# Optimization experiments

Measured on AMD Instinct MI355X. Metric: run time of the kernel, lower is better.

Reference implementation:

```python
import jax, jax.numpy as jnp
import numpy as np

# Standard NF4 quantization codebook (bitsandbytes values)
_NF4_CB = np.array([
    -1.0, -0.6961928009986877, -0.5250730514526367, -0.39491748809814453,
    -0.28444138169288635, -0.18477343022823334, -0.09105003625154495, 0.0,
    0.07958029955625534, 0.16093020141124725, 0.24611230194568634, 0.33791524171829224,
    0.44070982933044434, 0.5626170039176941, 0.7229568362236023, 1.0], dtype=np.float32)

B, L, H, E, DFF = 2, 2048, 2048, 8, 8192
BLK = 512  # NF4 quantization block size (b_idx = h // 512 in kernel)


def setup_inputs() -> dict:
    key = jax.random.key(0)
    ks = jax.random.split(key, 8)
    N = B * L
    x = jax.random.normal(ks[0], (B, L, H), dtype=jnp.float32)
    router_w = jax.random.normal(ks[1], (H, E), dtype=jnp.float32) * 0.02
    # packed NF4: one byte = two 4-bit codebook indices (low nibble -> even h)
    nf4 = jax.random.randint(ks[2], (N, E, H // 2), 0, 256, dtype=jnp.int32)
    mean = jax.random.normal(ks[3], (N, E, H // BLK), dtype=jnp.float32) * 0.01
    std = jax.random.uniform(ks[4], (N, E, H // BLK), dtype=jnp.float32) + 0.5
    codebook = jnp.asarray(_NF4_CB)
    w1 = jax.random.normal(ks[5], (H, DFF), dtype=jnp.float32) * 0.02
    w2 = jax.random.normal(ks[6], (DFF, H), dtype=jnp.float32) * 0.02
    return {"x": x, "router_w": router_w, "nf4": nf4, "mean": mean,
            "std": std, "codebook": codebook, "w1": w1, "w2": w2}


def reference(x, router_w, nf4, mean, std, codebook, w1, w2):
    b, l, h = x.shape
    n = b * l
    e = router_w.shape[1]
    xf = x.reshape(n, h)

    # shared expert MLP (base_mlp): Linear -> GELU -> Linear
    mlp = jax.nn.gelu(xf @ w1) @ w2  # [N, H]

    # router: logits in fp32, softmax, cast to fp16 as the kernel does
    logits = xf @ router_w  # [N, E]
    probs = jax.nn.softmax(logits, axis=-1).astype(jnp.float16).astype(jnp.float32)

    # NF4 unpack: low nibble -> even h, high nibble -> odd h
    low = nf4 & 15
    high = (nf4 >> 4) & 15
    idx = jnp.stack([low, high], axis=-1).reshape(n, e, h)  # interleave -> [N,E,H]
    vals = codebook[idx]  # codebook gather, [N,E,H]

    # per-block (512) rescale: val*std + mean
    nb = mean.shape[-1]
    blk = h // nb
    dq = (vals.reshape(n, e, nb, blk) * std[..., None] + mean[..., None]).reshape(n, e, h)

    # weighted expert mix + MLP residual add
    moe = jnp.einsum('ne,neh->nh', probs, dq)
    return (moe + mlp).reshape(b, l, h)
```

## Files before the change

### kernel.cpp

```cpp
#include <hip/hip_runtime.h>
#include <hip/hip_bf16.h>
#include <hip/hip_fp16.h>

#define H 2048
#define E 8
#define DFF 8192
#define NTOK 4096
#define NB 4

typedef _Float16 f16x8 __attribute__((ext_vector_type(8)));
typedef float f32x4 __attribute__((ext_vector_type(4)));

#define AS1 __attribute__((address_space(1)))
#define AS3 __attribute__((address_space(3)))

__device__ __forceinline__ void gl_lds16(const void* g, void* l) {
    __builtin_amdgcn_global_load_lds((const AS1 unsigned int*)g,
                                     (AS3 unsigned int*)l, 16, 0, 0);
}

__device__ __forceinline__ float gelu_f(float x) {
    float u = 0.7978845608028654f * x * (1.0f + 0.044715f * x * x);
    float t = fabsf(u);
    float e = __expf(-2.0f * t);
    float th = (1.0f - e) / (1.0f + e);
    th = copysignf(th, u);
    return 0.5f * x * (1.0f + th);
}

__global__ __launch_bounds__(256) void router_cast_kernel(
    const float* __restrict__ x, const float* __restrict__ rw,
    float* __restrict__ probs, _Float16* __restrict__ xh)
{
    int n = blockIdx.x, t = threadIdx.x;
    float acc[E];
#pragma unroll
    for (int e = 0; e < E; ++e) acc[e] = 0.f;
    const float* xr = x + (size_t)n * H;
#pragma unroll
    for (int k = 0; k < H / 256; ++k) {
        int h = t + k * 256;
        float xv = xr[h];
        xh[(size_t)n * H + h] = (_Float16)xv;
        const float4* r4 = reinterpret_cast<const float4*>(rw + (size_t)h * E);
        float4 a = r4[0], b = r4[1];
        acc[0] += xv * a.x; acc[1] += xv * a.y; acc[2] += xv * a.z; acc[3] += xv * a.w;
        acc[4] += xv * b.x; acc[5] += xv * b.y; acc[6] += xv * b.z; acc[7] += xv * b.w;
    }
#pragma unroll
    for (int e = 0; e < E; ++e) {
        float v = acc[e];
#pragma unroll
        for (int o = 32; o > 0; o >>= 1) v += __shfl_down(v, o, 64);
        acc[e] = v;
    }
    __shared__ float red[4][E];
    int wave = t >> 6, lane = t & 63;
    if (lane == 0) {
#pragma unroll
        for (int e = 0; e < E; ++e) red[wave][e] = acc[e];
    }
    __syncthreads();
    if (t == 0) {
        float lg[E];
        float mx = -1e30f;
#pragma unroll
        for (int e = 0; e < E; ++e) {
            lg[e] = red[0][e] + red[1][e] + red[2][e] + red[3][e];
            mx = fmaxf(mx, lg[e]);
        }
        float s = 0.f;
#pragma unroll
        for (int e = 0; e < E; ++e) { lg[e] = expf(lg[e] - mx); s += lg[e]; }
        float inv = 1.f / s;
#pragma unroll
        for (int e = 0; e < E; ++e) {
            float p = lg[e] * inv;
            p = __half2float(__float2half(p));
            probs[(size_t)n * E + e] = p;
        }
    }
}

__global__ __launch_bounds__(256) void transpose_cast_kernel(
    const float* __restrict__ src, _Float16* __restrict__ dst, int R, int C)
{
    __shared__ float tile[32][33];
    int tx = threadIdx.x & 31, ty = threadIdx.x >> 5;
    int c0 = blockIdx.x * 32, r0 = blockIdx.y * 32;
#pragma unroll
    for (int i = ty; i < 32; i += 8)
        tile[i][tx] = src[(size_t)(r0 + i) * C + c0 + tx];
    __syncthreads();
#pragma unroll
    for (int i = ty; i < 32; i += 8)
        dst[(size_t)(c0 + i) * R + r0 + tx] = (_Float16)tile[tx][i];
}

__global__ __launch_bounds__(256) void moe_kernel(
    const int* __restrict__ nf4, const float* __restrict__ mean,
    const float* __restrict__ stdv, const float* __restrict__ cb,
    const float* __restrict__ probs, float* __restrict__ moe)
{
    int n = blockIdx.x, t = threadIdx.x;
    __shared__ float cbl[32];
    __shared__ float ps[E][NB];
    __shared__ float cmean[NB];
    if (t < 16) { float v = cb[t]; cbl[t] = v; cbl[t + 16] = v; }
    else if (t >= 32 && t < 64) {
        int e = (t - 32) >> 2, b = t & 3;
        ps[e][b] = probs[(size_t)n * E + e] * stdv[((size_t)n * E + e) * NB + b];
    } else if (t >= 64 && t < 68) {
        int b = t - 64; float s = 0.f;
        for (int e = 0; e < E; ++e)
            s += probs[(size_t)n * E + e] * mean[((size_t)n * E + e) * NB + b];
        cmean[b] = s;
    }
    __syncthreads();
    int cboff = (t & 1) << 4;
    const int* w = nf4 + (size_t)n * (E * H / 2);
    float2* outp = reinterpret_cast<float2*>(moe + (size_t)n * H);
#pragma unroll
    for (int k = 0; k < 4; ++k) {
        int j = t + k * 256;
        float psr[E];
#pragma unroll
        for (int e = 0; e < E; ++e) psr[e] = ps[e][k];
        float cm = cmean[k];
        float aL = cm, aH = cm;
#pragma unroll
        for (int e = 0; e < E; ++e) {
            int word = w[e * (H / 2) + j];
            aL += psr[e] * cbl[(word & 15) + cboff];
            aH += psr[e] * cbl[((word >> 4) & 15) + cboff];
        }
        outp[j] = make_float2(aL, aH);
    }
}

template <int EPI, int BN, typename OT>
__global__ __launch_bounds__(512, 2) void gemm256_kernel(
    const _Float16* __restrict__ A, const _Float16* __restrict__ Bt,
    const float* __restrict__ addsrc, OT* __restrict__ outb,
    int K, int N, int bwShift)
{
    constexpr int BM = 256;
    constexpr int BK = 64;
    constexpr unsigned ASZ = BM * BK * 2;
    constexpr unsigned BSZ = BN * BK * 2;
    constexpr unsigned BUFSZ = ASZ + BSZ;
    constexpr int NLB = BSZ / 8192;
    constexpr int FI = (BN == 256) ? 8 : 4;
    constexpr int FIH = FI / 2;
    constexpr int SBS = (BN == 256) ? 16 : 32;

    __shared__ uint4 lds_u4[2 * BUFSZ / 16];
    char* lds = (char*)lds_u4;

    int t = threadIdx.x;
    int id = blockIdx.x;
    int xcd = id & 7, chunk = id >> 3;
    int bx = (xcd << bwShift) | (chunk & ((1 << bwShift) - 1));
    int by = chunk >> bwShift;
    int m0 = by * BM, n0 = bx * BN;

    const unsigned short* sA = (const unsigned short*)A
        + (size_t)(m0 + (t & (BM - 1))) * K + (t >> 8) * 8;
    const unsigned short* sB = (const unsigned short*)Bt
        + (size_t)(n0 + (t & (BN - 1))) * K + (t >> ((BN == 256) ? 8 : 7)) * 8;
    unsigned dstT = (unsigned)t * 16;

    int lane = t & 63, wave = t >> 6;
    int wr, wc;
    if constexpr (BN == 256) { wr = wave >> 2; wc = wave & 3; }
    else                     { wr = wave >> 1; wc = wave & 1; }
    int mb = wr * (FI * 16);
    int nb = wc * 64;
    int q = lane >> 4, m16 = lane & 15;

    f32x4 acc[FI][4] = {};
    f16x8 af[FI];
    f16x8 bh[2][4];

#pragma unroll
    for (int s = 0; s < 4; ++s)
        gl_lds16(sA + s * 16, lds + s * 8192 + dstT);
#pragma unroll
    for (int s = 0; s < NLB; ++s)
        gl_lds16(sB + s * SBS, lds + ASZ + s * 8192 + dstT);

    unsigned cur = 0;
    for (int k0 = 0; k0 < K; k0 += BK) {
        unsigned nxt = cur ^ BUFSZ;
        char* ldsR = lds + cur;
        char* ldsW = lds + nxt;
        bool more = (k0 + BK < K);
        int kn = k0 + BK;

        if (more) {
            gl_lds16(sA + kn,      ldsW + dstT);
            gl_lds16(sA + kn + 16, ldsW + 8192 + dstT);
            asm volatile("s_waitcnt vmcnt(2)" ::: "memory");
        } else {
            asm volatile("s_waitcnt vmcnt(0)" ::: "memory");
        }
        asm volatile("s_barrier" ::: "memory");
#pragma unroll
        for (int il = 0; il < FIH; ++il)
#pragma unroll
            for (int kh = 0; kh < 2; ++kh)
                af[il * 2 + kh] = *(const f16x8*)(ldsR +
                    (unsigned)((kh * 4 + q) * BM + mb + il * 16 + m16) * 16u);
#pragma unroll
        for (int jl = 0; jl < 2; ++jl)
#pragma unroll
            for (int kh = 0; kh < 2; ++kh)
                bh[0][jl * 2 + kh] = *(const f16x8*)(ldsR + ASZ +
                    (unsigned)((kh * 4 + q) * BN + nb + jl * 16 + m16) * 16u);
        __builtin_amdgcn_s_setprio(1);
#pragma unroll
        for (int il = 0; il < FIH; ++il)
#pragma unroll
            for (int jl = 0; jl < 2; ++jl)
#pragma unroll
                for (int kh = 0; kh < 2; ++kh)
                    acc[il][jl] = __builtin_amdgcn_mfma_f32_16x16x32_f16(
                        af[il * 2 + kh], bh[0][jl * 2 + kh], acc[il][jl], 0, 0, 0);
        __builtin_amdgcn_s_setprio(0);
        asm volatile("s_barrier" ::: "memory");

        if (more) {
            gl_lds16(sA + kn + 32, ldsW + 2 * 8192 + dstT);
            gl_lds16(sA + kn + 48, ldsW + 3 * 8192 + dstT);
        }
#pragma unroll
        for (int jl = 0; jl < 2; ++jl)
#pragma unroll
            for (int kh = 0; kh < 2; ++kh)
                bh[1][jl * 2 + kh] = *(const f16x8*)(ldsR + ASZ +
                    (unsigned)((kh * 4 + q) * BN + nb + (2 + jl) * 16 + m16) * 16u);
        __builtin_amdgcn_s_setprio(1);
#pragma unroll
        for (int il = 0; il < FIH; ++il)
#pragma unroll
            for (int jl = 0; jl < 2; ++jl)
#pragma unroll
                for (int kh = 0; kh < 2; ++kh)
                    acc[il][2 + jl] = __builtin_amdgcn_mfma_f32_16x16x32_f16(
                        af[il * 2 + kh], bh[1][jl * 2 + kh], acc[il][2 + jl], 0, 0, 0);
        __builtin_amdgcn_s_setprio(0);
        asm volatile("s_barrier" ::: "memory");

        if (more) {
            gl_lds16(sB + kn,       ldsW + ASZ + dstT);
            gl_lds16(sB + kn + SBS, ldsW + ASZ + 8192 + dstT);
        }
#pragma unroll
        for (int il = 0; il < FIH; ++il)
#pragma unroll
            for (int kh = 0; kh < 2; ++kh)
                af[il * 2 + kh] = *(const f16x8*)(ldsR +
                    (unsigned)((kh * 4 + q) * BM + mb + (FIH + il) * 16 + m16) * 16u);
        __builtin_amdgcn_s_setprio(1);
#pragma unroll
        for (int il = 0; il < FIH; ++il)
#pragma unroll
            for (int jl = 0; jl < 2; ++jl)
#pragma unroll
                for (int kh = 0; kh < 2; ++kh)
                    acc[FIH + il][2 + jl] = __builtin_amdgcn_mfma_f32_16x16x32_f16(
                        af[il * 2 + kh], bh[1][jl * 2 + kh], acc[FIH + il][2 + jl], 0, 0, 0);
        __builtin_amdgcn_s_setprio(0);
        asm volatile("s_barrier" ::: "memory");

        if constexpr (NLB == 4) {
            if (more) {
                gl_lds16(sB + kn + 2 * SBS, ldsW + ASZ + 2 * 8192 + dstT);
                gl_lds16(sB + kn + 3 * SBS, ldsW + ASZ + 3 * 8192 + dstT);
            }
        }
        __builtin_amdgcn_s_setprio(1);
#pragma unroll
        for (int il = 0; il < FIH; ++il)
#pragma unroll
            for (int jl = 0; jl < 2; ++jl)
#pragma unroll
                for (int kh = 0; kh < 2; ++kh)
                    acc[FIH + il][jl] = __builtin_amdgcn_mfma_f32_16x16x32_f16(
                        af[il * 2 + kh], bh[0][jl * 2 + kh], acc[FIH + il][jl], 0, 0, 0);
        __builtin_amdgcn_s_setprio(0);
        asm volatile("s_waitcnt lgkmcnt(0)" ::: "memory");
        asm volatile("s_barrier" ::: "memory");
        cur = nxt;
    }

#pragma unroll
    for (int i = 0; i < FI; ++i)
#pragma unroll
        for (int j = 0; j < 4; ++j) {
            int row = m0 + mb + i * 16 + q * 4;
            int col = n0 + nb + j * 16 + m16;
#pragma unroll
            for (int rix = 0; rix < 4; ++rix) {
                float v = acc[i][j][rix];
                size_t o = (size_t)(row + rix) * N + col;
                if constexpr (EPI == 0) {
                    outb[o] = (OT)gelu_f(v);
                } else {
                    outb[o] = (OT)(v + addsrc[o]);
                }
            }
        }
}

extern "C" void kernel_launch(void* const* d_in, const int* in_sizes, int n_in,
                              void* d_out, int out_size, void* d_ws, size_t ws_size,
                              hipStream_t stream) {
    const float* x    = (const float*)d_in[0];
    const float* rw   = (const float*)d_in[1];
    const int*   nf4  = (const int*)d_in[2];
    const float* mean = (const float*)d_in[3];
    const float* stdv = (const float*)d_in[4];
    const float* cb   = (const float*)d_in[5];
    const float* w1   = (const float*)d_in[6];
    const float* w2   = (const float*)d_in[7];
    float* out = (float*)d_out;

    char* ws = (char*)d_ws;
    float* probs      = (float*)ws;
    float* moe        = (float*)(ws + 131072);
    _Float16* xh      = (_Float16*)(ws + 33685504);
    _Float16* w1t     = (_Float16*)(ws + 50462720);
    _Float16* w2t     = (_Float16*)(ws + 84017152);
    _Float16* hid     = (_Float16*)(ws + 117571584);

    router_cast_kernel<<<NTOK, 256, 0, stream>>>(x, rw, probs, xh);
    transpose_cast_kernel<<<dim3(DFF / 32, H / 32), 256, 0, stream>>>(w1, w1t, H, DFF);
    transpose_cast_kernel<<<dim3(H / 32, DFF / 32), 256, 0, stream>>>(w2, w2t, DFF, H);
    moe_kernel<<<NTOK, 256, 0, stream>>>(nf4, mean, stdv, cb, probs, moe);
    gemm256_kernel<0, 256, _Float16><<<512, 512, 0, stream>>>(xh, w1t, nullptr, hid, H, DFF, 2);
    gemm256_kernel<1, 128, float><<<256, 512, 0, stream>>>(hid, w2t, moe, out, DFF, H, 1);
}
```

Baseline: 818.4 us.

## Triple-buffer GEMM LDS pipeline and use 256x128 tiles for first GEMM

Replaces the double-buffered LDS GEMM with a three-stage ring buffer that prefetches two K-steps ahead, so global loads have more time to land before they are consumed. The kernel is specialised to a 256x128 tile, which changes the first GEMM from 512 blocks of 256x256 to 1024 blocks of 256x128 with a different XCD swizzle. Narrower tiles lower arithmetic intensity per block, and the third buffer raises LDS use to 144KB, which could limit how many blocks fit per CU.

```diff
diff --git a/kernel.cpp b/kernel.cpp
--- a/kernel.cpp
+++ b/kernel.cpp
@@ -138,23 +138,21 @@
     }
 }
 
-template <int EPI, int BN, typename OT>
+template <int EPI, typename OT>
 __global__ __launch_bounds__(512, 2) void gemm256_kernel(
     const _Float16* __restrict__ A, const _Float16* __restrict__ Bt,
     const float* __restrict__ addsrc, OT* __restrict__ outb,
     int K, int N, int bwShift)
 {
     constexpr int BM = 256;
+    constexpr int BN = 128;
     constexpr int BK = 64;
     constexpr unsigned ASZ = BM * BK * 2;
     constexpr unsigned BSZ = BN * BK * 2;
     constexpr unsigned BUFSZ = ASZ + BSZ;
-    constexpr int NLB = BSZ / 8192;
-    constexpr int FI = (BN == 256) ? 8 : 4;
-    constexpr int FIH = FI / 2;
-    constexpr int SBS = (BN == 256) ? 16 : 32;
-
-    __shared__ uint4 lds_u4[2 * BUFSZ / 16];
+    constexpr unsigned LDSTOT = 3 * BUFSZ;
+
+    __shared__ uint4 lds_u4[LDSTOT / 16];
     char* lds = (char*)lds_u4;
 
     int t = threadIdx.x;
@@ -165,137 +163,143 @@
     int m0 = by * BM, n0 = bx * BN;
 
     const unsigned short* sA = (const unsigned short*)A
-        + (size_t)(m0 + (t & (BM - 1))) * K + (t >> 8) * 8;
+        + (size_t)(m0 + (t & 255)) * K + (t >> 8) * 8;
     const unsigned short* sB = (const unsigned short*)Bt
-        + (size_t)(n0 + (t & (BN - 1))) * K + (t >> ((BN == 256) ? 8 : 7)) * 8;
+        + (size_t)(n0 + (t & 127)) * K + (t >> 7) * 8;
     unsigned dstT = (unsigned)t * 16;
 
     int lane = t & 63, wave = t >> 6;
-    int wr, wc;
-    if constexpr (BN == 256) { wr = wave >> 2; wc = wave & 3; }
-    else                     { wr = wave >> 1; wc = wave & 1; }
-    int mb = wr * (FI * 16);
-    int nb = wc * 64;
+    int wr = wave >> 1, wc = wave & 1;
+    int mb = wr * 64, nb = wc * 64;
     int q = lane >> 4, m16 = lane & 15;
 
-    f32x4 acc[FI][4] = {};
-    f16x8 af[FI];
-    f16x8 bh[2][4];
-
-#pragma unroll
-    for (int s = 0; s < 4; ++s)
-        gl_lds16(sA + s * 16, lds + s * 8192 + dstT);
-#pragma unroll
-    for (int s = 0; s < NLB; ++s)
-        gl_lds16(sB + s * SBS, lds + ASZ + s * 8192 + dstT);
+    f32x4 acc[4][4] = {};
+    f16x8 af[4];
+    f16x8 bL[4];
+    f16x8 bH[4];
+
+#pragma unroll
+    for (int tl = 0; tl < 2; ++tl) {
+        char* W = lds + tl * BUFSZ;
+#pragma unroll
+        for (int s = 0; s < 4; ++s)
+            gl_lds16(sA + tl * BK + s * 16, W + s * 8192 + dstT);
+#pragma unroll
+        for (int s = 0; s < 2; ++s)
+            gl_lds16(sB + tl * BK + s * 32, W + ASZ + s * 8192 + dstT);
+    }
+    asm volatile("s_waitcnt vmcnt(6)" ::: "memory");
+    asm volatile("s_barrier" ::: "memory");
 
     unsigned cur = 0;
     for (int k0 = 0; k0 < K; k0 += BK) {
-        unsigned nxt = cur ^ BUFSZ;
-        char* ldsR = lds + cur;
-        char* ldsW = lds + nxt;
-        bool more = (k0 + BK < K);
-        int kn = k0 + BK;
-
-        if (more) {
-            gl_lds16(sA + kn,      ldsW + dstT);
-            gl_lds16(sA + kn + 16, ldsW + 8192 + dstT);
-            asm volatile("s_waitcnt vmcnt(2)" ::: "memory");
-        } else {
-            asm volatile("s_waitcnt vmcnt(0)" ::: "memory");
-        }
-        asm volatile("s_barrier" ::: "memory");
-#pragma unroll
-        for (int il = 0; il < FIH; ++il)
+        char* R = lds + cur;
+        unsigned stg = cur + 2 * BUFSZ;
+        if (stg >= LDSTOT) stg -= LDSTOT;
+        char* W = lds + stg;
+        bool st = (k0 + 2 * BK) < K;
+        int ks = k0 + 2 * BK;
+
+#pragma unroll
+        for (int il = 0; il < 2; ++il)
 #pragma unroll
             for (int kh = 0; kh < 2; ++kh)
-                af[il * 2 + kh] = *(const f16x8*)(ldsR +
+                af[il * 2 + kh] = *(const f16x8*)(R +
                     (unsigned)((kh * 4 + q) * BM + mb + il * 16 + m16) * 16u);
 #pragma unroll
         for (int jl = 0; jl < 2; ++jl)
 #pragma unroll
             for (int kh = 0; kh < 2; ++kh)
-                bh[0][jl * 2 + kh] = *(const f16x8*)(ldsR + ASZ +
+                bL[jl * 2 + kh] = *(const f16x8*)(R + ASZ +
                     (unsigned)((kh * 4 + q) * BN + nb + jl * 16 + m16) * 16u);
+        if (st) {
+            gl_lds16(sA + ks,      W + dstT);
+            gl_lds16(sA + ks + 16, W + 8192 + dstT);
+        }
+        asm volatile("s_barrier" ::: "memory");
+        asm volatile("s_waitcnt lgkmcnt(0)" ::: "memory");
         __builtin_amdgcn_s_setprio(1);
 #pragma unroll
-        for (int il = 0; il < FIH; ++il)
+        for (int il = 0; il < 2; ++il)
 #pragma unroll
             for (int jl = 0; jl < 2; ++jl)
 #pragma unroll
                 for (int kh = 0; kh < 2; ++kh)
                     acc[il][jl] = __builtin_amdgcn_mfma_f32_16x16x32_f16(
-                        af[il * 2 + kh], bh[0][jl * 2 + kh], acc[il][jl], 0, 0, 0);
+                        af[il * 2 + kh], bL[jl * 2 + kh], acc[il][jl], 0, 0, 0);
         __builtin_amdgcn_s_setprio(0);
         asm volatile("s_barrier" ::: "memory");
 
-        if (more) {
-            gl_lds16(sA + kn + 32, ldsW + 2 * 8192 + dstT);
-            gl_lds16(sA + kn + 48, ldsW + 3 * 8192 + dstT);
-        }
 #pragma unroll
         for (int jl = 0; jl < 2; ++jl)
 #pragma unroll
             for (int kh = 0; kh < 2; ++kh)
-                bh[1][jl * 2 + kh] = *(const f16x8*)(ldsR + ASZ +
+                bH[jl * 2 + kh] = *(const f16x8*)(R + ASZ +
                     (unsigned)((kh * 4 + q) * BN + nb + (2 + jl) * 16 + m16) * 16u);
+        if (st) {
+            gl_lds16(sA + ks + 32, W + 2 * 8192 + dstT);
+            gl_lds16(sA + ks + 48, W + 3 * 8192 + dstT);
+        }
+        asm volatile("s_barrier" ::: "memory");
+        asm volatile("s_waitcnt lgkmcnt(0)" ::: "memory");
         __builtin_amdgcn_s_setprio(1);
 #pragma unroll
-        for (int il = 0; il < FIH; ++il)
+        for (int il = 0; il < 2; ++il)
 #pragma unroll
             for (int jl = 0; jl < 2; ++jl)
 #pragma unroll
                 for (int kh = 0; kh < 2; ++kh)
                     acc[il][2 + jl] = __builtin_amdgcn_mfma_f32_16x16x32_f16(
-                        af[il * 2 + kh], bh[1][jl * 2 + kh], acc[il][2 + jl], 0, 0, 0);
+                        af[il * 2 + kh], bH[jl * 2 + kh], acc[il][2 + jl], 0, 0, 0);
         __builtin_amdgcn_s_setprio(0);
         asm volatile("s_barrier" ::: "memory");
 
-        if (more) {
-            gl_lds16(sB + kn,       ldsW + ASZ + dstT);
-            gl_lds16(sB + kn + SBS, ldsW + ASZ + 8192 + dstT);
-        }
-#pragma unroll
-        for (int il = 0; il < FIH; ++il)
+#pragma unroll
+        for (int il = 0; il < 2; ++il)
 #pragma unroll
             for (int kh = 0; kh < 2; ++kh)
-                af[il * 2 + kh] = *(const f16x8*)(ldsR +
-                    (unsigned)((kh * 4 + q) * BM + mb + (FIH + il) * 16 + m16) * 16u);
+                af[il * 2 + kh] = *(const f16x8*)(R +
+                    (unsigned)((kh * 4 + q) * BM + mb + (2 + il) * 16 + m16) * 16u);
+        if (st) {
+            gl_lds16(sB + ks,      W + ASZ + dstT);
+            gl_lds16(sB + ks + 32, W + ASZ + 8192 + dstT);
+        }
+        asm volatile("s_barrier" ::: "memory");
+        asm volatile("s_waitcnt lgkmcnt(0)" ::: "memory");
         __builtin_amdgcn_s_setprio(1);
 #pragma unroll
-        for (int il = 0; il < FIH; ++il)
+        for (int il = 0; il < 2; ++il)
 #pragma unroll
             for (int jl = 0; jl < 2; ++jl)
 #pragma unroll
                 for (int kh = 0; kh < 2; ++kh)
-                    acc[FIH + il][2 + jl] = __builtin_amdgcn_mfma_f32_16x16x32_f16(
-                        af[il * 2 + kh], bh[1][jl * 2 + kh], acc[FIH + il][2 + jl], 0, 0, 0);
+                    acc[2 + il][2 + jl] = __builtin_amdgcn_mfma_f32_16x16x32_f16(
+                        af[il * 2 + kh], bH[jl * 2 + kh], acc[2 + il][2 + jl], 0, 0, 0);
         __builtin_amdgcn_s_setprio(0);
         asm volatile("s_barrier" ::: "memory");
 
-        if constexpr (NLB == 4) {
-            if (more) {
-                gl_lds16(sB + kn + 2 * SBS, ldsW + ASZ + 2 * 8192 + dstT);
-                gl_lds16(sB + kn + 3 * SBS, ldsW + ASZ + 3 * 8192 + dstT);
-            }
-        }
         __builtin_amdgcn_s_setprio(1);
 #pragma unroll
-        for (int il = 0; il < FIH; ++il)
+        for (int il = 0; il < 2; ++il)
 #pragma unroll
             for (int jl = 0; jl < 2; ++jl)
 #pragma unroll
                 for (int kh = 0; kh < 2; ++kh)
-                    acc[FIH + il][jl] = __builtin_amdgcn_mfma_f32_16x16x32_f16(
-                        af[il * 2 + kh], bh[0][jl * 2 + kh], acc[FIH + il][jl], 0, 0, 0);
+                    acc[2 + il][jl] = __builtin_amdgcn_mfma_f32_16x16x32_f16(
+                        af[il * 2 + kh], bL[jl * 2 + kh], acc[2 + il][jl], 0, 0, 0);
         __builtin_amdgcn_s_setprio(0);
-        asm volatile("s_waitcnt lgkmcnt(0)" ::: "memory");
-        asm volatile("s_barrier" ::: "memory");
-        cur = nxt;
-    }
-
-#pragma unroll
-    for (int i = 0; i < FI; ++i)
+        if (st)
+            asm volatile("s_waitcnt vmcnt(6)" ::: "memory");
+        else
+            asm volatile("s_waitcnt vmcnt(0)" ::: "memory");
+        asm volatile("s_barrier" ::: "memory");
+
+        cur += BUFSZ;
+        if (cur >= LDSTOT) cur -= LDSTOT;
+    }
+
+#pragma unroll
+    for (int i = 0; i < 4; ++i)
 #pragma unroll
         for (int j = 0; j < 4; ++j) {
             int row = m0 + mb + i * 16 + q * 4;
@@ -338,6 +342,6 @@
     transpose_cast_kernel<<<dim3(DFF / 32, H / 32), 256, 0, stream>>>(w1, w1t, H, DFF);
     transpose_cast_kernel<<<dim3(H / 32, DFF / 32), 256, 0, stream>>>(w2, w2t, DFF, H);
     moe_kernel<<<NTOK, 256, 0, stream>>>(nf4, mean, stdv, cb, probs, moe);
-    gemm256_kernel<0, 256, _Float16><<<512, 512, 0, stream>>>(xh, w1t, nullptr, hid, H, DFF, 2);
-    gemm256_kernel<1, 128, float><<<256, 512, 0, stream>>>(hid, w2t, moe, out, DFF, H, 1);
-}
+    gemm256_kernel<0, _Float16><<<1024, 512, 0, stream>>>(xh, w1t, nullptr, hid, H, DFF, 3);
+    gemm256_kernel<1, float><<<256, 512, 0, stream>>>(hid, w2t, moe, out, DFF, H, 1);
+}
```

Result: slower. 872.9 us (+6.7%).
